# Performance work log

Measured on AMD Instinct MI355X. Metric: run time of the kernel, lower is better.

The kernel has to match this reference:

```python
import jax, jax.numpy as jnp
import numpy as np

B, S, D, H, FF = 2, 2048, 1024, 16, 4096
DH = D // H
EPS = 1e-5


def _linear_params(key, din, dout):
    kw, kb = jax.random.split(key)
    lim = 1.0 / np.sqrt(din)
    W = jax.random.uniform(kw, (din, dout), jnp.float32, -lim, lim)
    b = jax.random.uniform(kb, (dout,), jnp.float32, -lim, lim)
    return W, b


def setup_inputs() -> dict:
    key = jax.random.key(0)
    ks = jax.random.split(key, 8)
    x = jax.random.normal(ks[0], (B, S, D), jnp.float32)
    mask = jnp.ones((B, 1, 1, S), jnp.int32)
    wq, bq = _linear_params(ks[1], D, D)
    wk, bk = _linear_params(ks[2], D, D)
    wv, bv = _linear_params(ks[3], D, D)
    w1, b1 = _linear_params(ks[4], D, D)       # linear1 (attn output proj)
    fw1, fb1 = _linear_params(ks[5], D, FF)    # ffn.w_1
    fw2, fb2 = _linear_params(ks[6], FF, D)    # ffn.w_2
    g1 = jnp.ones((D,), jnp.float32); be1 = jnp.zeros((D,), jnp.float32)
    g2 = jnp.ones((D,), jnp.float32); be2 = jnp.zeros((D,), jnp.float32)
    return dict(x=x, mask=mask, wq=wq, bq=bq, wk=wk, bk=bk, wv=wv, bv=bv,
                w1=w1, b1=b1, g1=g1, be1=be1,
                fw1=fw1, fb1=fb1, fw2=fw2, fb2=fb2, g2=g2, be2=be2)


def _layernorm(x, g, b):
    mu = jnp.mean(x, axis=-1, keepdims=True)
    var = jnp.mean(jnp.square(x - mu), axis=-1, keepdims=True)
    return (x - mu) * jax.lax.rsqrt(var + EPS) * g + b


def _encoder(x, mask, wq, bq, wk, bk, wv, bv, w1, b1, g1, be1,
             fw1, fb1, fw2, fb2, g2, be2):
    res = x
    # QKV projections, reshape to [B, H, S, DH]
    q = (x @ wq + bq).reshape(B, S, H, DH).transpose(0, 2, 1, 3)
    k = (x @ wk + bk).reshape(B, S, H, DH).transpose(0, 2, 1, 3)
    v = (x @ wv + bv).reshape(B, S, H, DH).transpose(0, 2, 1, 3)
    scores = jnp.einsum('bhqd,bhkd->bhqk', q, k) / np.sqrt(DH).astype(np.float32)
    scores = jnp.where(mask == 0, jnp.float32(-1e9), scores)
    probs = jax.nn.softmax(scores, axis=-1)  # dropout = identity in eval
    attn = jnp.einsum('bhqk,bhkd->bhqd', probs, v)
    attn = attn.transpose(0, 2, 1, 3).reshape(B, S, D)
    x = _layernorm(attn @ w1 + b1 + res, g1, be1)
    res = x
    ff = jax.nn.relu(x @ fw1 + fb1) @ fw2 + fb2
    return _layernorm(ff + res, g2, be2)


def reference(x, mask, wq, bq, wk, bk, wv, bv, w1, b1, g1, be1,
              fw1, fb1, fw2, fb2, g2, be2):
    return _encoder(x, mask, wq, bq, wk, bk, wv, bv, w1, b1, g1, be1,
                    fw1, fb1, fw2, fb2, g2, be2)
```

## Files before the change

### kernel.cpp

```cpp
#include <hip/hip_runtime.h>
#include <hip/hip_bf16.h>
#include <cstdint>

typedef unsigned short u16;
typedef __attribute__((ext_vector_type(8))) short bf16x8;
typedef __attribute__((ext_vector_type(4))) float f32x4;

#define DEVFN static __device__ __forceinline__

static constexpr int S    = 2048;
static constexpr int D    = 1024;
static constexpr int DHd  = 64;
static constexpr int FFd  = 4096;
static constexpr int M    = 4096;
static constexpr int LDQK = 2048;

static constexpr float SC2 = 0.18033688f;

DEVFN u16 f2b(float v) {
    union { __hip_bfloat16 h; u16 u; } x;
    x.h = __float2bfloat16(v);
    return x.u;
}
DEVFN float b2f(u16 u) {
    union { float f; uint32_t i; } x;
    x.i = ((uint32_t)u) << 16;
    return x.f;
}

typedef const uint32_t __attribute__((address_space(1)))* gptr_t;
typedef uint32_t __attribute__((address_space(3)))* lptr_t;
DEVFN void load16(const void* g, void* l) {
    __builtin_amdgcn_global_load_lds((gptr_t)g, (lptr_t)l, 16, 0, 0);
}

template<int MODE, int KS>
__global__ __launch_bounds__(512, 2)
void gemm256(const u16* __restrict__ A, const u16* __restrict__ BT,
             const float* __restrict__ bias, void* __restrict__ outp,
             u16* __restrict__ vout, int N)
{
    __shared__ __align__(16) u16 Lds[65536];
    const int tid  = threadIdx.x;
    const int lane = tid & 63;
    const int w    = tid >> 6;
    const int wm = w >> 2, wn = w & 3;
    const int g = lane >> 4, c = lane & 15;
    const int c7 = c & 7;
    const int bn0 = blockIdx.x * 256;
    const int bm0 = blockIdx.y * 256;
    const int z   = (MODE == 4) ? (int)blockIdx.z : 0;
    const size_t kofs = (size_t)z * 1024;

    const int sr = tid >> 3;
    const int gl = (tid & 7) ^ (sr & 7);
    const u16* Asrc = A  + (size_t)(bm0 + sr) * KS + kofs + gl * 8;
    const u16* Bsrc = BT + (size_t)(bn0 + sr) * KS + kofs + gl * 8;
    char* dA = (char*)Lds + (size_t)tid * 16;
    char* dB = dA + 32768;

#define STG_A(BUF, H, KT)                                                       \
    { _Pragma("unroll") for (int Lh = 0; Lh < 2; ++Lh)                          \
        load16(Asrc + (size_t)((H)*128 + Lh*64) * KS + (KT)*64,                 \
               dA + (BUF)*65536 + (H)*16384 + Lh*8192); }
#define STG_B(BUF, H, KT)                                                       \
    { _Pragma("unroll") for (int Lh = 0; Lh < 2; ++Lh)                          \
        load16(Bsrc + (size_t)((H)*128 + Lh*64) * KS + (KT)*64,                 \
               dB + (BUF)*65536 + (H)*16384 + Lh*8192); }
#define VMCNT(N_) asm volatile("s_waitcnt vmcnt(" #N_ ")" ::: "memory")
#define BAR() { __builtin_amdgcn_s_barrier(); __builtin_amdgcn_sched_barrier(0); }

    const char* lbase = (const char*)Lds;
    auto rdA = [&](int buf, int i, int kk) -> bf16x8 {
        const int half = i >> 2;
        const int lr = (2*(i & 3) + wm) * 16 + c;
        return *(const bf16x8*)(lbase + buf*65536 + half*16384 + lr*128
                                + (((kk<<2) + g) ^ c7) * 16);
    };
    auto rdB = [&](int buf, int j, int kk) -> bf16x8 {
        const int half = j >> 1;
        const int lr = (j & 1)*64 + wn*16 + c;
        return *(const bf16x8*)(lbase + buf*65536 + 32768 + half*16384 + lr*128
                                + (((kk<<2) + g) ^ c7) * 16);
    };

    const f32x4 fz = {0.f, 0.f, 0.f, 0.f};
    f32x4 acc[8][4];
#pragma unroll
    for (int i = 0; i < 8; ++i)
#pragma unroll
        for (int j = 0; j < 4; ++j) acc[i][j] = fz;

    bf16x8 af[4][2], bf[4][2];

    auto body = [&](int cur, int nxt, int kt, bool stage) {
        if (stage) STG_A(nxt, 0, kt + 1);
#pragma unroll
        for (int i = 0; i < 4; ++i)
#pragma unroll
            for (int kk = 0; kk < 2; ++kk) af[i][kk] = rdA(cur, i, kk);
#pragma unroll
        for (int j = 0; j < 2; ++j)
#pragma unroll
            for (int kk = 0; kk < 2; ++kk) bf[j][kk] = rdB(cur, j, kk);
        __builtin_amdgcn_s_setprio(1);
#pragma unroll
        for (int i = 0; i < 4; ++i)
#pragma unroll
            for (int j = 0; j < 2; ++j)
#pragma unroll
                for (int kk = 0; kk < 2; ++kk)
                    acc[i][j] = __builtin_amdgcn_mfma_f32_16x16x32_bf16(
                        af[i][kk], bf[j][kk], acc[i][j], 0, 0, 0);
        __builtin_amdgcn_s_setprio(0);
        if (stage) { VMCNT(4); } else { VMCNT(2); }
        BAR();
        if (stage) STG_B(nxt, 0, kt + 1);
#pragma unroll
        for (int j = 2; j < 4; ++j)
#pragma unroll
            for (int kk = 0; kk < 2; ++kk) bf[j][kk] = rdB(cur, j, kk);
        __builtin_amdgcn_s_setprio(1);
#pragma unroll
        for (int i = 0; i < 4; ++i)
#pragma unroll
            for (int j = 2; j < 4; ++j)
#pragma unroll
                for (int kk = 0; kk < 2; ++kk)
                    acc[i][j] = __builtin_amdgcn_mfma_f32_16x16x32_bf16(
                        af[i][kk], bf[j][kk], acc[i][j], 0, 0, 0);
        __builtin_amdgcn_s_setprio(0);
        if (stage) { VMCNT(4); } else { VMCNT(0); }
        BAR();
        if (stage) STG_B(nxt, 1, kt + 1);
#pragma unroll
        for (int i = 4; i < 8; ++i)
#pragma unroll
            for (int kk = 0; kk < 2; ++kk) af[i - 4][kk] = rdA(cur, i, kk);
        __builtin_amdgcn_s_setprio(1);
#pragma unroll
        for (int i = 4; i < 8; ++i)
#pragma unroll
            for (int j = 0; j < 2; ++j)
#pragma unroll
                for (int kk = 0; kk < 2; ++kk)
                    acc[i][j] = __builtin_amdgcn_mfma_f32_16x16x32_bf16(
                        af[i - 4][kk], bf[j][kk], acc[i][j], 0, 0, 0);
        __builtin_amdgcn_s_setprio(0);
        if (stage) STG_A(nxt, 1, kt + 1);
        __builtin_amdgcn_s_setprio(1);
#pragma unroll
        for (int i = 4; i < 8; ++i)
#pragma unroll
            for (int j = 2; j < 4; ++j)
#pragma unroll
                for (int kk = 0; kk < 2; ++kk)
                    acc[i][j] = __builtin_amdgcn_mfma_f32_16x16x32_bf16(
                        af[i - 4][kk], bf[j][kk], acc[i][j], 0, 0, 0);
        __builtin_amdgcn_s_setprio(0);
        if (stage) { VMCNT(4); BAR(); }
    };

    STG_A(0, 0, 0); STG_B(0, 0, 0); STG_B(0, 1, 0); STG_A(0, 1, 0);
    VMCNT(4);
    BAR();

#pragma unroll 1
    for (int kt = 0; kt < 14; kt += 2) {
        body(0, 1, kt, true);
        body(1, 0, kt + 1, true);
    }
    body(0, 1, 14, true);
    body(1, 0, 15, false);
#undef STG_A
#undef STG_B
#undef VMCNT
#undef BAR

#pragma unroll
    for (int i = 0; i < 8; ++i) {
        const int fm = (i >> 2) * 8 + (i & 3) * 2 + wm;
        const int row = bm0 + fm * 16 + 4 * g;
#pragma unroll
        for (int j = 0; j < 4; ++j) {
            const int fn = (j >> 1) * 8 + (j & 1) * 4 + wn;
            const int col = bn0 + fn * 16 + c;
            if (MODE == 4) {
                u16* outz = (u16*)outp + (size_t)z * M * D;
#pragma unroll
                for (int r = 0; r < 4; ++r)
                    outz[(size_t)(row + r) * D + col] = f2b(acc[i][j][r]);
            } else if (MODE == 3 && col >= 2048) {
                const float bv = bias[col];
                union { u16 u[4]; uint2 v; } pk;
#pragma unroll
                for (int r = 0; r < 4; ++r) pk.u[r] = f2b(acc[i][j][r] + bv);
                const size_t vidx = ((size_t)(row >> 11) * 1024 + (col - 2048))
                                    * (size_t)S + (row & 2047);
                *(uint2*)&vout[vidx] = pk.v;
            } else {
                const float bv = bias[col];
                const float sc = (MODE == 3 && col < D) ? SC2 : 1.f;
                const int nn = (MODE == 3) ? LDQK : N;
#pragma unroll
                for (int r = 0; r < 4; ++r) {
                    float v = acc[i][j][r] + bv;
                    if (MODE == 2) v = v > 0.f ? v : 0.f;
                    v *= sc;
                    ((u16*)outp)[(size_t)(row + r) * nn + col] = f2b(v);
                }
            }
        }
    }
}

template<int KTOT>
__global__ __launch_bounds__(256, 3)
void gemm_splitk(const u16* __restrict__ A, const u16* __restrict__ BT,
                 u16* __restrict__ part)
{
    __shared__ __align__(16) u16 As[128 * 64];
    __shared__ __align__(16) u16 Bs[128 * 64];
    const int tid  = threadIdx.x;
    const int lane = tid & 63;
    const int w    = tid >> 6;
    const int wm = w >> 1, wn = w & 1;
    const int g = lane >> 4, c = lane & 15;
    const int bn0 = blockIdx.x * 128;
    const int bm0 = blockIdx.y * 128;
    const int z   = blockIdx.z;
    const int srow = tid >> 3;
    const int scol = (tid & 7) * 8;

    const f32x4 fz = {0.f, 0.f, 0.f, 0.f};
    f32x4 acc[4][4];
#pragma unroll
    for (int i = 0; i < 4; ++i)
#pragma unroll
        for (int j = 0; j < 4; ++j) acc[i][j] = fz;

    const u16* Ab = A  + (size_t)(bm0 + srow) * KTOT + z * (KTOT/2) + scol;
    const u16* Bb = BT + (size_t)(bn0 + srow) * KTOT + z * (KTOT/2) + scol;
    char* AsB = (char*)As + (size_t)tid * 16;
    char* BsB = (char*)Bs + (size_t)tid * 16;

    for (int kt = 0; kt < KTOT/128; ++kt) {
        const int k0 = kt << 6;
        __syncthreads();
#pragma unroll
        for (int cc = 0; cc < 4; ++cc) {
            load16(Ab + (size_t)(cc * 32) * KTOT + k0, AsB + cc * 4096);
            load16(Bb + (size_t)(cc * 32) * KTOT + k0, BsB + cc * 4096);
        }
        __syncthreads();
#pragma unroll
        for (int kk = 0; kk < 2; ++kk) {
            bf16x8 af[4], bfv[4];
#pragma unroll
            for (int i = 0; i < 4; ++i)
                af[i] = *(const bf16x8*)&As[(wm*64 + i*16 + c) * 64 + kk*32 + g*8];
#pragma unroll
            for (int j = 0; j < 4; ++j)
                bfv[j] = *(const bf16x8*)&Bs[(wn*64 + j*16 + c) * 64 + kk*32 + g*8];
#pragma unroll
            for (int i = 0; i < 4; ++i)
#pragma unroll
                for (int j = 0; j < 4; ++j)
                    acc[i][j] = __builtin_amdgcn_mfma_f32_16x16x32_bf16(
                        af[i], bfv[j], acc[i][j], 0, 0, 0);
        }
    }

    u16* outz = part + (size_t)z * M * D;
#pragma unroll
    for (int i = 0; i < 4; ++i) {
        const int row = bm0 + wm*64 + i*16 + g*4;
#pragma unroll
        for (int j = 0; j < 4; ++j) {
            const int col = bn0 + wn*64 + j*16 + c;
#pragma unroll
            for (int r = 0; r < 4; ++r)
                outz[(size_t)(row + r) * D + col] = f2b(acc[i][j][r]);
        }
    }
}

template<int NPART, bool BRES>
__global__ __launch_bounds__(256)
void ln_part_fused(const u16* __restrict__ part, const float* __restrict__ bias,
                   const float* __restrict__ residf, const u16* __restrict__ residb,
                   const float* __restrict__ gam, const float* __restrict__ bet,
                   u16* __restrict__ out_b, float* __restrict__ out_f)
{
    const int row = blockIdx.x;
    const int tid = threadIdx.x;
    __shared__ float red1[4], red2[4];
    const float4 bv = ((const float4*)bias)[tid];
    float y0 = bv.x, y1 = bv.y, y2 = bv.z, y3 = bv.w;
    if (BRES) {
        union { u16 u[4]; uint2 v; } rk;
        rk.v = *(const uint2*)&residb[(size_t)row * D + tid * 4];
        y0 += b2f(rk.u[0]); y1 += b2f(rk.u[1]);
        y2 += b2f(rk.u[2]); y3 += b2f(rk.u[3]);
    } else {
        const float4 rv = ((const float4*)(residf + (size_t)row * D))[tid];
        y0 += rv.x; y1 += rv.y; y2 += rv.z; y3 += rv.w;
    }
#pragma unroll
    for (int p = 0; p < NPART; ++p) {
        union { u16 u[4]; uint2 v; } pk;
        pk.v = *(const uint2*)&part[(size_t)(p * M + row) * D + tid * 4];
        y0 += b2f(pk.u[0]); y1 += b2f(pk.u[1]);
        y2 += b2f(pk.u[2]); y3 += b2f(pk.u[3]);
    }
    float s1 = y0 + y1 + y2 + y3;
#pragma unroll
    for (int off = 1; off < 64; off <<= 1) s1 += __shfl_xor(s1, off);
    if ((tid & 63) == 0) red1[tid >> 6] = s1;
    __syncthreads();
    const float mu = (red1[0] + red1[1] + red1[2] + red1[3]) * (1.f / 1024.f);
    const float d0 = y0 - mu, d1 = y1 - mu, d2 = y2 - mu, d3 = y3 - mu;
    float s2 = d0*d0 + d1*d1 + d2*d2 + d3*d3;
#pragma unroll
    for (int off = 1; off < 64; off <<= 1) s2 += __shfl_xor(s2, off);
    if ((tid & 63) == 0) red2[tid >> 6] = s2;
    __syncthreads();
    const float var = (red2[0] + red2[1] + red2[2] + red2[3]) * (1.f / 1024.f);
    const float rs = rsqrtf(var + 1e-5f);
    const int c0 = tid * 4;
    const float o0 = d0 * rs * gam[c0+0] + bet[c0+0];
    const float o1 = d1 * rs * gam[c0+1] + bet[c0+1];
    const float o2 = d2 * rs * gam[c0+2] + bet[c0+2];
    const float o3 = d3 * rs * gam[c0+3] + bet[c0+3];
    if (out_b) {
        union { u16 u[4]; uint2 v; } pk;
        pk.u[0] = f2b(o0); pk.u[1] = f2b(o1); pk.u[2] = f2b(o2); pk.u[3] = f2b(o3);
        ((uint2*)(out_b + (size_t)row * D))[tid] = pk.v;
    }
    if (out_f) {
        float4 yv; yv.x = o0; yv.y = o1; yv.z = o2; yv.w = o3;
        ((float4*)(out_f + (size_t)row * D))[tid] = yv;
    }
}

__global__ __launch_bounds__(256, 3)
void attn_fwd11(const u16* __restrict__ QK, const u16* __restrict__ VT,
                u16* __restrict__ Op, float* __restrict__ Lp)
{
    __shared__ __align__(16) u16 Ks[2][64 * 64];
    __shared__ __align__(16) u16 Vs[2][64 * 64];
    __shared__ __align__(16) u16 Ps[4][32 * 72];
    const int tid  = threadIdx.x;
    const int lane = tid & 63;
    const int w    = tid >> 6;
    const int g = lane >> 4, c = lane & 15;

    int wid = (int)blockIdx.x;
    wid = (wid & 7) * 128 + (wid >> 3);
    const int bh   = wid >> 5;
    const int half = (wid >> 4) & 1;
    const int qt   = wid & 15;
    const int b = bh >> 4, h = bh & 15;
    const int q0 = qt * 128 + w * 32;
    const int kt0 = half * 16;

    const u16* Qb = QK;
    const u16* Kb = QK + 1024;

    bf16x8 aq[2][2];
#pragma unroll
    for (int rt = 0; rt < 2; ++rt)
#pragma unroll
        for (int kk = 0; kk < 2; ++kk)
            aq[rt][kk] = *(const bf16x8*)&Qb[(size_t)(b*S + q0 + rt*16 + c) * LDQK
                                             + h*DHd + kk*32 + g*8];

    const f32x4 fz = {0.f, 0.f, 0.f, 0.f};
    const short one_b = (short)0x3F80;
    const bf16x8 onesv = {one_b, one_b, one_b, one_b, one_b, one_b, one_b, one_b};
    f32x4 o[2][4];
    f32x4 ol[2];
#pragma unroll
    for (int rt = 0; rt < 2; ++rt) {
        ol[rt] = fz;
#pragma unroll
        for (int j = 0; j < 4; ++j) o[rt][j] = fz;
    }

    const int sr = tid >> 3;
    const int glog = (tid & 7) ^ (sr & 7);
    const u16* Ksrc = Kb + (size_t)(b*S + sr) * LDQK + h*DHd + glog*8;
    const u16* Vsrc = VT + (size_t)(bh*DHd + sr) * S + glog*8;
    char* Kd0 = (char*)&Ks[0][0] + (size_t)tid * 16;
    char* Vd0 = (char*)&Vs[0][0] + (size_t)tid * 16;

#define STAGE(BUFI, kt_)                                                        \
    {                                                                           \
        const int kr0_ = (kt_) * 64;                                            \
        _Pragma("unroll")                                                       \
        for (int cc = 0; cc < 2; ++cc) {                                        \
            load16(Ksrc + (size_t)(kr0_ + cc*32) * LDQK, Kd0 + (BUFI)*8192 + cc*4096); \
            load16(Vsrc + (size_t)(cc*32) * S + kr0_,    Vd0 + (BUFI)*8192 + cc*4096); \
        }                                                                       \
    }
#define WAITBAR(N)                                                              \
    {                                                                           \
        asm volatile("s_waitcnt vmcnt(" #N ")" ::: "memory");                   \
        __builtin_amdgcn_s_barrier();                                           \
        __builtin_amdgcn_sched_barrier(0);                                      \
    }

    u16* pw = &Ps[w][0];
    const int c7 = c & 7;

    auto tile_body = [&](const u16* K0, const u16* V0) {
        bf16x8 bk[4][2];
#pragma unroll
        for (int j = 0; j < 4; ++j)
#pragma unroll
            for (int kk = 0; kk < 2; ++kk)
                bk[j][kk] = *(const bf16x8*)&K0[(j*16 + c) * 64 + (((kk<<2)+g) ^ c7) * 8];

#pragma unroll
        for (int rt = 0; rt < 2; ++rt) {
            f32x4 sv[4];
            __builtin_amdgcn_s_setprio(1);
#pragma unroll
            for (int j = 0; j < 4; ++j) {
                sv[j] = fz;
#pragma unroll
                for (int kk = 0; kk < 2; ++kk)
                    sv[j] = __builtin_amdgcn_mfma_f32_16x16x32_bf16(
                        bk[j][kk], aq[rt][kk], sv[j], 0, 0, 0);
            }
            __builtin_amdgcn_s_setprio(0);

#pragma unroll
            for (int j = 0; j < 4; ++j) {
                const float p0 = exp2f(sv[j][0]);
                const float p1 = exp2f(sv[j][1]);
                const float p2 = exp2f(sv[j][2]);
                const float p3 = exp2f(sv[j][3]);
                union { u16 u[4]; uint2 v; } pk;
                pk.u[0] = f2b(p0); pk.u[1] = f2b(p1);
                pk.u[2] = f2b(p2); pk.u[3] = f2b(p3);
                *(uint2*)&pw[(rt*16 + c) * 72 + j*16 + g*4] = pk.v;
            }
        }

        __builtin_amdgcn_s_setprio(1);
#pragma unroll
        for (int st = 0; st < 2; ++st) {
            bf16x8 bv[4];
#pragma unroll
            for (int j = 0; j < 4; ++j)
                bv[j] = *(const bf16x8*)&V0[(j*16 + c) * 64 + (((st<<2)+g) ^ c7) * 8];
#pragma unroll
            for (int rt = 0; rt < 2; ++rt) {
                const bf16x8 ap = *(const bf16x8*)&pw[(rt*16 + c) * 72 + st*32 + g*8];
#pragma unroll
                for (int j = 0; j < 4; ++j)
                    o[rt][j] = __builtin_amdgcn_mfma_f32_16x16x32_bf16(
                        ap, bv[j], o[rt][j], 0, 0, 0);
                ol[rt] = __builtin_amdgcn_mfma_f32_16x16x32_bf16(
                    ap, onesv, ol[rt], 0, 0, 0);
            }
        }
        __builtin_amdgcn_s_setprio(0);
    };

    STAGE(0, kt0);
    WAITBAR(0);
#pragma unroll 1
    for (int it = 0; it < 7; ++it) {
        STAGE(1, kt0 + 2*it + 1); tile_body(&Ks[0][0], &Vs[0][0]); WAITBAR(0);
        STAGE(0, kt0 + 2*it + 2); tile_body(&Ks[1][0], &Vs[1][0]); WAITBAR(0);
    }
    STAGE(1, kt0 + 15); tile_body(&Ks[0][0], &Vs[0][0]); WAITBAR(0);
    tile_body(&Ks[1][0], &Vs[1][0]);
#undef STAGE
#undef WAITBAR

    u16* Oz = Op + (size_t)half * M * D;
    float* Lz = Lp + (size_t)(half * 16 + h) * M;
#pragma unroll
    for (int rt = 0; rt < 2; ++rt) {
#pragma unroll
        for (int r = 0; r < 4; ++r) {
            const int grow = b*S + q0 + rt*16 + 4*g + r;
            if (c == 0) Lz[grow] = ol[rt][r];
            const size_t rowo = (size_t)grow * D + h*DHd;
#pragma unroll
            for (int j = 0; j < 4; ++j)
                Oz[rowo + j*16 + c] = f2b(o[rt][j][r]);
        }
    }
}

__global__ __launch_bounds__(256)
void attn_merge(const u16* __restrict__ Op, const float* __restrict__ Lp,
                u16* __restrict__ Ob)
{
    const int idx = blockIdx.x * 256 + threadIdx.x;
    const int m   = idx >> 7;
    const int col = (idx & 127) * 8;
    const int h   = col >> 6;
    const float rl = __builtin_amdgcn_rcpf(Lp[(size_t)h*M + m] +
                                           Lp[(size_t)(16+h)*M + m]);
    union { u16 u[8]; uint4 v; } pa, pb, po;
    pa.v = *(const uint4*)&Op[(size_t)m*D + col];
    pb.v = *(const uint4*)&Op[(size_t)(M + m)*D + col];
#pragma unroll
    for (int r = 0; r < 8; ++r)
        po.u[r] = f2b((b2f(pa.u[r]) + b2f(pb.u[r])) * rl);
    *(uint4*)&Ob[(size_t)m*D + col] = po.v;
}

__global__ __launch_bounds__(256)
void prep_all_k(const float* __restrict__ x,
                const float* __restrict__ wq, const float* __restrict__ wk,
                const float* __restrict__ wv, const float* __restrict__ w1,
                const float* __restrict__ fw1, const float* __restrict__ fw2,
                const float* __restrict__ bq, const float* __restrict__ bk,
                const float* __restrict__ bv, u16* __restrict__ Xb,
                u16* __restrict__ WqkvT, u16* __restrict__ W1T,
                u16* __restrict__ F1T, u16* __restrict__ F2T,
                float* __restrict__ bqkv)
{
    __shared__ float tile[32][33];
    int blk = blockIdx.x;
    if (blk < 4096) {
        const int i = blk * 256 + threadIdx.x;
        const float4 v = ((const float4*)x)[i];
        union { u16 u[4]; uint2 p; } pk;
        pk.u[0] = f2b(v.x); pk.u[1] = f2b(v.y);
        pk.u[2] = f2b(v.z); pk.u[3] = f2b(v.w);
        ((uint2*)Xb)[i] = pk.p;
        return;
    }
    blk -= 4096;
    if (blk >= 12288) {
        const int i = (blk - 12288) * 256 + threadIdx.x;
        bqkv[i] = i < 1024 ? bq[i] : (i < 2048 ? bk[i - 1024] : bv[i - 2048]);
        return;
    }
    const float* src; u16* dst; int R, C, c0, r0;
    if (blk < 3072) {
        const int z = blk >> 10, t = blk & 1023;
        src = z == 0 ? wq : (z == 1 ? wk : wv);
        dst = WqkvT + (size_t)z * D * D;
        R = D; C = D; c0 = (t & 31) * 32; r0 = (t >> 5) * 32;
    } else if (blk < 4096) {
        const int t = blk - 3072;
        src = w1; dst = W1T;
        R = D; C = D; c0 = (t & 31) * 32; r0 = (t >> 5) * 32;
    } else if (blk < 8192) {
        const int t = blk - 4096;
        src = fw1; dst = F1T;
        R = D; C = FFd; c0 = (t & 127) * 32; r0 = (t >> 7) * 32;
    } else {
        const int t = blk - 8192;
        src = fw2; dst = F2T;
        R = FFd; C = D; c0 = (t & 31) * 32; r0 = (t >> 5) * 32;
    }
    const int tx = threadIdx.x & 31, ty = threadIdx.x >> 5;
#pragma unroll
    for (int i = 0; i < 4; ++i)
        tile[ty + i*8][tx] = src[(size_t)(r0 + ty + i*8) * C + c0 + tx];
    __syncthreads();
#pragma unroll
    for (int i = 0; i < 4; ++i)
        dst[(size_t)(c0 + ty + i*8) * R + r0 + tx] = f2b(tile[tx][ty + i*8]);
}

extern "C" void kernel_launch(void* const* d_in, const int* in_sizes, int n_in,
                              void* d_out, int out_size, void* d_ws, size_t ws_size,
                              hipStream_t stream)
{
    (void)in_sizes; (void)n_in; (void)out_size; (void)ws_size;
    const float* x   = (const float*)d_in[0];
    const float* wq  = (const float*)d_in[2];
    const float* bq  = (const float*)d_in[3];
    const float* wk  = (const float*)d_in[4];
    const float* bk  = (const float*)d_in[5];
    const float* wv  = (const float*)d_in[6];
    const float* bv  = (const float*)d_in[7];
    const float* w1  = (const float*)d_in[8];
    const float* b1  = (const float*)d_in[9];
    const float* g1  = (const float*)d_in[10];
    const float* be1 = (const float*)d_in[11];
    const float* fw1 = (const float*)d_in[12];
    const float* fb1 = (const float*)d_in[13];
    const float* fw2 = (const float*)d_in[14];
    const float* fb2 = (const float*)d_in[15];
    const float* g2  = (const float*)d_in[16];
    const float* be2 = (const float*)d_in[17];

    char* ws = (char*)d_ws;
    size_t off = 0;
    auto alloc = [&](size_t bytes) -> void* {
        void* p = ws + off;
        off += (bytes + 255) & ~(size_t)255;
        return p;
    };
    u16*   QKb   = (u16*)alloc((size_t)M * LDQK * 2);
    u16*   VTh   = (u16*)alloc((size_t)M * D * 2);
    u16*   Ob    = (u16*)alloc((size_t)M * D * 2);
    u16*   Xb    = (u16*)alloc((size_t)M * D * 2);
    u16*   WqkvT = (u16*)alloc((size_t)3 * D * D * 2);
    u16*   W1T   = (u16*)alloc((size_t)D * D * 2);
    u16*   F1T   = (u16*)alloc((size_t)D * FFd * 2);
    u16*   F2T   = (u16*)alloc((size_t)D * FFd * 2);
    u16*   x1b   = (u16*)alloc((size_t)M * D * 2);
    u16*   Hb    = (u16*)alloc((size_t)M * FFd * 2);
    float* bqkv  = (float*)alloc((size_t)3 * D * 4);

    u16*   Part = QKb;
    u16*   Opart = Hb;
    float* Lpart = (float*)(Hb + (size_t)2 * M * D);

    prep_all_k<<<dim3(16396), dim3(256), 0, stream>>>(
        x, wq, wk, wv, w1, fw1, fw2, bq, bk, bv,
        Xb, WqkvT, W1T, F1T, F2T, bqkv);

    gemm256<3, D><<<dim3(3 * D / 256, M/256), 512, 0, stream>>>(
        Xb, WqkvT, bqkv, QKb, VTh, LDQK);

    attn_fwd11<<<dim3(1024), 256, 0, stream>>>(QKb, VTh, Opart, Lpart);
    attn_merge<<<dim3(2048), 256, 0, stream>>>(Opart, Lpart, Ob);

    gemm_splitk<D><<<dim3(D/128, M/128, 2), 256, 0, stream>>>(Ob, W1T, Part);

    ln_part_fused<2, false><<<dim3(M), 256, 0, stream>>>(
        Part, b1, x, nullptr, g1, be1, x1b, nullptr);

    gemm256<2, D><<<dim3(FFd/256, M/256), 512, 0, stream>>>(
        x1b, F1T, fb1, Hb, nullptr, FFd);

    gemm256<4, FFd><<<dim3(D/256, M/256, 4), 512, 0, stream>>>(
        Hb, F2T, nullptr, Part, nullptr, D);

    ln_part_fused<4, true><<<dim3(M), 256, 0, stream>>>(
        Part, fb2, nullptr, x1b, g2, be2, nullptr, (float*)d_out);
}
```

Measured before the change: 221.1 us.

## Fuse attention split-K merge into attention kernel via last-block atomic flag

Removes the separate attn_merge launch. Each attention block increments a per-(batch,head,qtile) counter after writing its partial output and row sums. The second block to arrive merges both halves and writes the normalized bf16 output. The counters are zeroed in an extra block of the prep kernel. This saves a kernel launch and a full pass over the partial buffers, but adds fences, an atomic, and a serialized merge tail in the last-arriving blocks.

```diff
diff --git a/kernel.cpp b/kernel.cpp
--- a/kernel.cpp
+++ b/kernel.cpp
@@ -344,8 +344,9 @@
 }
 
 __global__ __launch_bounds__(256, 3)
-void attn_fwd11(const u16* __restrict__ QK, const u16* __restrict__ VT,
-                u16* __restrict__ Op, float* __restrict__ Lp)
+void attn_fwd13(const u16* __restrict__ QK, const u16* __restrict__ VT,
+                u16* __restrict__ Op, float* __restrict__ Lp,
+                u16* __restrict__ Ob, uint32_t* __restrict__ flags)
 {
     __shared__ __align__(16) u16 Ks[2][64 * 64];
     __shared__ __align__(16) u16 Vs[2][64 * 64];
@@ -363,6 +364,7 @@
     const int b = bh >> 4, h = bh & 15;
     const int q0 = qt * 128 + w * 32;
     const int kt0 = half * 16;
+    const int pair = bh * 16 + qt;
 
     const u16* Qb = QK;
     const u16* Kb = QK + 1024;
@@ -495,25 +497,36 @@
                 Oz[rowo + j*16 + c] = f2b(o[rt][j][r]);
         }
     }
-}
-
-__global__ __launch_bounds__(256)
-void attn_merge(const u16* __restrict__ Op, const float* __restrict__ Lp,
-                u16* __restrict__ Ob)
-{
-    const int idx = blockIdx.x * 256 + threadIdx.x;
-    const int m   = idx >> 7;
-    const int col = (idx & 127) * 8;
-    const int h   = col >> 6;
-    const float rl = __builtin_amdgcn_rcpf(Lp[(size_t)h*M + m] +
-                                           Lp[(size_t)(16+h)*M + m]);
-    union { u16 u[8]; uint4 v; } pa, pb, po;
-    pa.v = *(const uint4*)&Op[(size_t)m*D + col];
-    pb.v = *(const uint4*)&Op[(size_t)(M + m)*D + col];
-#pragma unroll
-    for (int r = 0; r < 8; ++r)
-        po.u[r] = f2b((b2f(pa.u[r]) + b2f(pb.u[r])) * rl);
-    *(uint4*)&Ob[(size_t)m*D + col] = po.v;
+
+    __threadfence();
+    __syncthreads();
+    __shared__ int amLast;
+    if (tid == 0) {
+        const uint32_t old = atomicAdd(&flags[pair], 1u);
+        amLast = (old == 1u);
+    }
+    __syncthreads();
+    if (amLast) {
+        __threadfence();
+        const float* L0 = Lp + (size_t)h * M;
+        const float* L1 = Lp + (size_t)(16 + h) * M;
+#pragma unroll
+        for (int t = 0; t < 4; ++t) {
+            const int task = t * 256 + tid;
+            const int r  = task >> 3;
+            const int cg = (task & 7) * 8;
+            const int m  = b*S + qt*128 + r;
+            const float rl = __builtin_amdgcn_rcpf(L0[m] + L1[m]);
+            const size_t base = (size_t)m * D + h*DHd + cg;
+            union { u16 u[8]; uint4 v; } pa, pb, po;
+            pa.v = *(const uint4*)&Op[base];
+            pb.v = *(const uint4*)&Op[(size_t)M * D + base];
+#pragma unroll
+            for (int e = 0; e < 8; ++e)
+                po.u[e] = f2b((b2f(pa.u[e]) + b2f(pb.u[e])) * rl);
+            *(uint4*)&Ob[base] = po.v;
+        }
+    }
 }
 
 __global__ __launch_bounds__(256)
@@ -525,7 +538,7 @@
                 const float* __restrict__ bv, u16* __restrict__ Xb,
                 u16* __restrict__ WqkvT, u16* __restrict__ W1T,
                 u16* __restrict__ F1T, u16* __restrict__ F2T,
-                float* __restrict__ bqkv)
+                float* __restrict__ bqkv, uint32_t* __restrict__ flags)
 {
     __shared__ float tile[32][33];
     int blk = blockIdx.x;
@@ -539,6 +552,11 @@
         return;
     }
     blk -= 4096;
+    if (blk == 12300) {
+        flags[threadIdx.x] = 0u;
+        flags[threadIdx.x + 256] = 0u;
+        return;
+    }
     if (blk >= 12288) {
         const int i = (blk - 12288) * 256 + threadIdx.x;
         bqkv[i] = i < 1024 ? bq[i] : (i < 2048 ? bk[i - 1024] : bv[i - 2048]);
@@ -614,20 +632,20 @@
     u16*   x1b   = (u16*)alloc((size_t)M * D * 2);
     u16*   Hb    = (u16*)alloc((size_t)M * FFd * 2);
     float* bqkv  = (float*)alloc((size_t)3 * D * 4);
+    uint32_t* flags = (uint32_t*)alloc(512 * 4);
 
     u16*   Part = QKb;
     u16*   Opart = Hb;
     float* Lpart = (float*)(Hb + (size_t)2 * M * D);
 
-    prep_all_k<<<dim3(16396), dim3(256), 0, stream>>>(
+    prep_all_k<<<dim3(16397), dim3(256), 0, stream>>>(
         x, wq, wk, wv, w1, fw1, fw2, bq, bk, bv,
-        Xb, WqkvT, W1T, F1T, F2T, bqkv);
+        Xb, WqkvT, W1T, F1T, F2T, bqkv, flags);
 
     gemm256<3, D><<<dim3(3 * D / 256, M/256), 512, 0, stream>>>(
         Xb, WqkvT, bqkv, QKb, VTh, LDQK);
 
-    attn_fwd11<<<dim3(1024), 256, 0, stream>>>(QKb, VTh, Opart, Lpart);
-    attn_merge<<<dim3(2048), 256, 0, stream>>>(Opart, Lpart, Ob);
+    attn_fwd13<<<dim3(1024), 256, 0, stream>>>(QKb, VTh, Opart, Lpart, Ob, flags);
 
     gemm_splitk<D><<<dim3(D/128, M/128, 2), 256, 0, stream>>>(Ob, W1T, Part);
 
```

Result: slower. 389.9 us (+76.3%).
